# Optimization experiments

Measured on AMD Instinct MI355X. Metric: run time of the kernel, lower is better.

The kernel has to match this reference:

```python
import jax, jax.numpy as jnp
import numpy as np

B=4; TEXT_LEN=64; IMG=256; P=16; DIM=1024; HEADS=16; LAYERS=2; MLP=4; VOCAB=50000; TDIM=256; MAXTXT=2048
HP=IMG//P; NPATCH=HP*HP; HD=DIM//HEADS; EPS=1e-5

def _ln(x, g, b):
    m = jnp.mean(x, -1, keepdims=True)
    v = jnp.mean((x - m) ** 2, -1, keepdims=True)
    return (x - m) / jnp.sqrt(v + EPS) * g + b

def _rope_cos_sin(n, d):
    inv = 1.0 / (10000.0 ** (jnp.arange(0, d, 2, dtype=jnp.float32) / d))
    f = jnp.outer(jnp.arange(n, dtype=jnp.float32), inv)
    e = jnp.concatenate([f, f], -1)  # [n, d]
    return jnp.cos(e), jnp.sin(e)

def _rot_half(x):
    # matches torch: cat((-x[...,1::2], x[...,::2]), -1)
    return jnp.concatenate([-x[..., 1::2], x[..., ::2]], -1)

def _forward(noisy_images, text_tokens, timesteps, W_tok, pos_text, W_patch, pos_img, cls_tok,
             W_t1, b_t1, W_t2, b_t2, ln1_g, ln1_b, Wq, Wk, Wv, Wo, ln2_g, ln2_b,
             Wm1, Wm2, Wada, b_ada, fn_g, fn_b, W_final, b_final):
    Bn = noisy_images.shape[0]
    # text embed: one_hot @ W_tok.T == gather of columns of W_tok [DIM, VOCAB]
    text_emb = jnp.transpose(jnp.take(W_tok, text_tokens, axis=1), (1, 2, 0)) + pos_text[:, :TEXT_LEN]
    # image patches: [B,3,HP,P,HP,P] -> [B,HP,WP,C,P,P] -> [B,NPATCH, 3*P*P]
    patches = noisy_images.reshape(Bn, 3, HP, P, HP, P).transpose(0, 2, 4, 1, 3, 5).reshape(Bn, NPATCH, 3 * P * P)
    img_emb = patches @ W_patch.T + pos_img
    img_emb = jnp.concatenate([jnp.broadcast_to(cls_tok, (Bn, 1, DIM)), img_emb], 1)
    x = jnp.concatenate([text_emb, img_emb], 1)  # [B, N, DIM]
    N = x.shape[1]
    # sinusoidal timestep embedding (dim=256)
    half = TDIM // 2
    freqs = jnp.exp(-jnp.log(10000.0) * jnp.arange(half, dtype=jnp.float32) / half)
    args = timesteps.astype(jnp.float32)[:, None] * freqs[None]
    temb_raw = jnp.concatenate([jnp.cos(args), jnp.sin(args)], -1)
    t_emb = jax.nn.silu(temb_raw @ W_t1.T + b_t1) @ W_t2.T + b_t2  # [B, DIM]
    cos, sin = _rope_cos_sin(N, HD)
    scale = HD ** -0.5
    for l in range(LAYERS):
        mod = jax.nn.silu(t_emb) @ Wada[l].T + b_ada[l]
        sh_msa, sc_msa, g_msa, sh_mlp, sc_mlp, g_mlp = jnp.split(mod, 6, -1)
        xn = _ln(x, ln1_g[l], ln1_b[l]) * (1 + sc_msa[:, None]) + sh_msa[:, None]
        q = (xn @ Wq[l].T).reshape(Bn, N, HEADS, HD).transpose(0, 2, 1, 3)
        k = (xn @ Wk[l].T).reshape(Bn, N, HEADS, HD).transpose(0, 2, 1, 3)
        v = (xn @ Wv[l].T).reshape(Bn, N, HEADS, HD).transpose(0, 2, 1, 3)
        q = q * cos + _rot_half(q) * sin
        k = k * cos + _rot_half(k) * sin
        att = jax.nn.softmax(jnp.einsum('bhnd,bhmd->bhnm', q, k) * scale, -1)
        o = jnp.einsum('bhnm,bhmd->bhnd', att, v).transpose(0, 2, 1, 3).reshape(Bn, N, DIM)
        x = x + g_msa[:, None] * (o @ Wo[l].T)
        xn2 = _ln(x, ln2_g[l], ln2_b[l]) * (1 + sc_mlp[:, None]) + sh_mlp[:, None]
        mlp = jax.nn.gelu(xn2 @ Wm1[l].T, approximate=False) @ Wm2[l].T
        x = x + g_mlp[:, None] * mlp
    img_tok = x[:, TEXT_LEN + 1:]
    out = _ln(img_tok, fn_g, fn_b) @ W_final.T + b_final  # [B, NPATCH, 3*P*P]
    out = out.reshape(Bn, HP, HP, 3, P, P).transpose(0, 3, 1, 4, 2, 5).reshape(Bn, 3, IMG, IMG)
    return out

def setup_inputs() -> dict:
    key = jax.random.key(0)
    ks = jax.random.split(key, 24)
    def n(k, shape, s=0.02):
        return (jax.random.normal(k, shape, jnp.float32) * s).astype(jnp.float32)
    inp = {}
    inp['noisy_images'] = jax.random.normal(ks[0], (B, 3, IMG, IMG), jnp.float32)
    inp['text_tokens'] = jax.random.randint(ks[1], (B, TEXT_LEN), 0, VOCAB)
    inp['timesteps'] = jax.random.randint(ks[2], (B,), 0, 1000)
    inp['W_tok'] = n(ks[3], (DIM, VOCAB))
    inp['pos_text'] = n(ks[4], (1, MAXTXT, DIM))
    inp['W_patch'] = n(ks[5], (DIM, 3 * P * P))
    inp['pos_img'] = n(ks[6], (1, NPATCH, DIM))
    inp['cls_tok'] = n(ks[7], (1, 1, DIM))
    inp['W_t1'] = n(ks[8], (DIM, TDIM)); inp['b_t1'] = jnp.zeros((DIM,), jnp.float32)
    inp['W_t2'] = n(ks[9], (DIM, DIM)); inp['b_t2'] = jnp.zeros((DIM,), jnp.float32)
    inp['ln1_g'] = jnp.ones((LAYERS, DIM), jnp.float32); inp['ln1_b'] = jnp.zeros((LAYERS, DIM), jnp.float32)
    inp['Wq'] = n(ks[10], (LAYERS, DIM, DIM))
    inp['Wk'] = n(ks[11], (LAYERS, DIM, DIM))
    inp['Wv'] = n(ks[12], (LAYERS, DIM, DIM))
    inp['Wo'] = n(ks[13], (LAYERS, DIM, DIM))
    inp['ln2_g'] = jnp.ones((LAYERS, DIM), jnp.float32); inp['ln2_b'] = jnp.zeros((LAYERS, DIM), jnp.float32)
    inp['Wm1'] = n(ks[14], (LAYERS, MLP * DIM, DIM))
    inp['Wm2'] = n(ks[15], (LAYERS, DIM, MLP * DIM))
    inp['Wada'] = n(ks[16], (LAYERS, 6 * DIM, DIM)); inp['b_ada'] = jnp.zeros((LAYERS, 6 * DIM), jnp.float32)
    inp['fn_g'] = jnp.ones((DIM,), jnp.float32); inp['fn_b'] = jnp.zeros((DIM,), jnp.float32)
    inp['W_final'] = n(ks[17], (3 * P * P, DIM)); inp['b_final'] = jnp.zeros((3 * P * P,), jnp.float32)
    return inp

def reference(noisy_images, text_tokens, timesteps, W_tok, pos_text, W_patch, pos_img, cls_tok,
              W_t1, b_t1, W_t2, b_t2, ln1_g, ln1_b, Wq, Wk, Wv, Wo, ln2_g, ln2_b,
              Wm1, Wm2, Wada, b_ada, fn_g, fn_b, W_final, b_final):
    return _forward(noisy_images, text_tokens, timesteps, W_tok, pos_text, W_patch, pos_img, cls_tok,
                    W_t1, b_t1, W_t2, b_t2, ln1_g, ln1_b, Wq, Wk, Wv, Wo, ln2_g, ln2_b,
                    Wm1, Wm2, Wada, b_ada, fn_g, fn_b, W_final, b_final)
```

## Files before the change

### kernel.cpp

```cpp
#include <hip/hip_runtime.h>
#include <math.h>

constexpr int kBn    = 4;
constexpr int kText  = 64;
constexpr int kImg   = 256;
constexpr int kDim   = 1024;
constexpr int kHeads = 16;
constexpr int kHd    = 64;
constexpr int kNp    = 256;
constexpr int kTok   = 321;
constexpr int kVocab = 50000;
constexpr int kTdim  = 256;
constexpr int kMlp   = 4096;
constexpr int kScLd  = 328;
constexpr float kEps = 1e-5f;

typedef __attribute__((ext_vector_type(8))) short short8;
typedef __attribute__((ext_vector_type(4))) float f32x4;

__device__ __forceinline__ short f2bf(float x) {
  unsigned u = __builtin_bit_cast(unsigned, x);
  unsigned r = (u + 0x7FFFu + ((u >> 16) & 1u)) >> 16;
  return (short)r;
}

__device__ __forceinline__ void glds16(const short* g, short* l) {
  __builtin_amdgcn_global_load_lds(
      (const __attribute__((address_space(1))) unsigned int*)g,
      (__attribute__((address_space(3))) unsigned int*)l, 16, 0, 0);
}

struct GemmM {
  const short* A; const short* B; float* C; const float* E;
  int M, N, K, lda, ldb, ldc;
  long sA0, sA1, sB0, sB1, sC0, sC1;
  int innerB, ldE, rowsPB;
  float alpha;
  int nSplit, splitLen;
  long partStride;
};

__device__ __forceinline__ float epi_apply(int EPI, const GemmM& p, const float* E,
                                           long co, int gm, int gn, float v) {
  if (EPI == 1) v += E[gn];
  else if (EPI == 3) v = 0.5f*v*(1.f + erff(v*0.70710678118654752f));
  else if (EPI == 4) v += E[(long)gm*p.ldE + gn];
  else if (EPI == 5) v = p.C[co] + E[(long)(gm / p.rowsPB)*p.ldE + gn] * v;
  return v;
}

template<int EPI, bool PART, bool OUTBF>
__global__ __launch_bounds__(256) void gemm_gl(GemmM p) {
  int bz = blockIdx.z;
  int split = 0;
  if (PART) { split = bz % p.nSplit; bz /= p.nSplit; }
  int b1 = bz % p.innerB, b0 = bz / p.innerB;
  const short* A = p.A + b0*p.sA0 + b1*p.sA1;
  const short* B = p.B + b0*p.sB0 + b1*p.sB1;
  long cbase = b0*p.sC0 + b1*p.sC1 + (PART ? (long)split * p.partStride : 0);
  const float* E = p.E;

  int kBeg = PART ? split * p.splitLen : 0;
  int kEnd = PART ? min(p.K, kBeg + p.splitLen) : p.K;

  __shared__ short As[2][64*64];
  __shared__ short Bs[2][64*64];

  int tid  = threadIdx.x;
  int lane = tid & 63, widx = tid >> 6;
  int quad = lane >> 4, ln = lane & 15;
  int wm = (widx >> 1) * 32, wn = (widx & 1) * 32;
  int n0 = blockIdx.x * 64, m0 = blockIdx.y * 64;

  int l3 = lane >> 3, l7 = lane & 7;
  int kofs = (l7 ^ l3) * 8;
  const short* gA0 = A + (long)(m0 + 16*widx + l3) * p.lda + kofs;
  const short* gA1 = gA0 + (long)8 * p.lda;
  const short* gB0 = B + (long)(n0 + 16*widx + l3) * p.ldb + kofs;
  const short* gB1 = gB0 + (long)8 * p.ldb;
  short* lA0 = &As[0][(2*widx)*512];
  short* lA1 = &As[0][(2*widx+1)*512];
  short* lB0 = &Bs[0][(2*widx)*512];
  short* lB1 = &Bs[0][(2*widx+1)*512];

  auto stage = [&](int buf, int k0) {
    int bo = buf * 4096;
    glds16(gA0 + k0, lA0 + bo);
    glds16(gA1 + k0, lA1 + bo);
    glds16(gB0 + k0, lB0 + bo);
    glds16(gB1 + k0, lB1 + bo);
  };

  f32x4 zero = {0.f, 0.f, 0.f, 0.f};
  f32x4 acc[2][2];
  acc[0][0] = zero; acc[0][1] = zero; acc[1][0] = zero; acc[1][1] = zero;

  stage(0, kBeg);
  int buf = 0;
  for (int k0 = kBeg; k0 < kEnd; k0 += 64) {
    if (k0 + 64 < kEnd) stage(buf ^ 1, k0 + 64);
    __syncthreads();
    const char* Ab = (const char*)&As[buf][0];
    const char* Bb = (const char*)&Bs[buf][0];
#pragma unroll
    for (int ks = 0; ks < 2; ++ks) {
      int cb = ks*64 + quad*16;
      int r0 = wm + ln, r1 = wm + 16 + ln, r2 = wn + ln, r3 = wn + 16 + ln;
      short8 a0 = *(const short8*)(Ab + r0*128 + (cb ^ ((r0 & 7) << 4)));
      short8 a1 = *(const short8*)(Ab + r1*128 + (cb ^ ((r1 & 7) << 4)));
      short8 b0 = *(const short8*)(Bb + r2*128 + (cb ^ ((r2 & 7) << 4)));
      short8 b1 = *(const short8*)(Bb + r3*128 + (cb ^ ((r3 & 7) << 4)));
      acc[0][0] = __builtin_amdgcn_mfma_f32_16x16x32_bf16(a0, b0, acc[0][0], 0, 0, 0);
      acc[0][1] = __builtin_amdgcn_mfma_f32_16x16x32_bf16(a0, b1, acc[0][1], 0, 0, 0);
      acc[1][0] = __builtin_amdgcn_mfma_f32_16x16x32_bf16(a1, b0, acc[1][0], 0, 0, 0);
      acc[1][1] = __builtin_amdgcn_mfma_f32_16x16x32_bf16(a1, b1, acc[1][1], 0, 0, 0);
    }
    __syncthreads();
    buf ^= 1;
  }

#pragma unroll
  for (int mi = 0; mi < 2; ++mi)
#pragma unroll
    for (int ni = 0; ni < 2; ++ni)
#pragma unroll
      for (int reg = 0; reg < 4; ++reg) {
        int gm = m0 + wm + mi*16 + quad*4 + reg;
        int gn = n0 + wn + ni*16 + ln;
        if (gm >= p.M || gn >= p.N) continue;
        long co = cbase + (long)gm * p.ldc + gn;
        float v = acc[mi][ni][reg] * p.alpha;
        if (!PART) v = epi_apply(EPI, p, E, co, gm, gn, v);
        if (OUTBF) ((short*)p.C)[co] = f2bf(v);
        else       p.C[co] = v;
      }
}

template<int EPI, bool OUTBF>
__global__ __launch_bounds__(256) void gemm_mfma(GemmM p) {
  int bz = blockIdx.z;
  int b1 = bz % p.innerB, b0 = bz / p.innerB;
  const short* A = p.A + b0*p.sA0 + b1*p.sA1;
  const short* B = p.B + b0*p.sB0 + b1*p.sB1;
  long cbase = b0*p.sC0 + b1*p.sC1;
  const float* E = p.E;
  int kEnd = p.K;

  __shared__ short As[64*72];
  __shared__ short Bs[64*72];

  int tid  = threadIdx.x;
  int lane = tid & 63, widx = tid >> 6;
  int quad = lane >> 4, ln = lane & 15;
  int wm = (widx >> 1) * 32, wn = (widx & 1) * 32;
  int n0 = blockIdx.x * 64, m0 = blockIdx.y * 64;

  f32x4 zero = {0.f, 0.f, 0.f, 0.f};
  f32x4 acc[2][2];
  acc[0][0] = zero; acc[0][1] = zero; acc[1][0] = zero; acc[1][1] = zero;

  short8 ra[2], rb[2];
  auto issueLoads = [&](int k0) {
#pragma unroll
    for (int r = 0; r < 2; ++r) {
      int c = tid + 256*r;
      int row = c >> 3, kc = c & 7;
      int gk = k0 + kc*8;
      {
        int gm = m0 + row;
        const short* src = A + (long)gm * p.lda + gk;
        if (gm < p.M && gk + 8 <= kEnd) ra[r] = *(const short8*)src;
        else {
          short8 t = {0,0,0,0,0,0,0,0};
          if (gm < p.M) {
#pragma unroll
            for (int j = 0; j < 8; ++j) if (gk + j < kEnd) t[j] = src[j];
          }
          ra[r] = t;
        }
      }
      {
        int gn = n0 + row;
        const short* src = B + (long)gn * p.ldb + gk;
        if (gn < p.N && gk + 8 <= kEnd) rb[r] = *(const short8*)src;
        else {
          short8 t = {0,0,0,0,0,0,0,0};
          if (gn < p.N) {
#pragma unroll
            for (int j = 0; j < 8; ++j) if (gk + j < kEnd) t[j] = src[j];
          }
          rb[r] = t;
        }
      }
    }
  };

  issueLoads(0);
  for (int k0 = 0; k0 < kEnd; k0 += 64) {
#pragma unroll
    for (int r = 0; r < 2; ++r) {
      int c = tid + 256*r;
      int row = c >> 3, kc = c & 7;
      *(short8*)&As[row*72 + kc*8] = ra[r];
      *(short8*)&Bs[row*72 + kc*8] = rb[r];
    }
    __syncthreads();
    if (k0 + 64 < kEnd) issueLoads(k0 + 64);
#pragma unroll
    for (int ks = 0; ks < 2; ++ks) {
      short8 a0 = *(const short8*)&As[(wm +      ln)*72 + ks*32 + quad*8];
      short8 a1 = *(const short8*)&As[(wm + 16 + ln)*72 + ks*32 + quad*8];
      short8 b0 = *(const short8*)&Bs[(wn +      ln)*72 + ks*32 + quad*8];
      short8 b1 = *(const short8*)&Bs[(wn + 16 + ln)*72 + ks*32 + quad*8];
      acc[0][0] = __builtin_amdgcn_mfma_f32_16x16x32_bf16(a0, b0, acc[0][0], 0, 0, 0);
      acc[0][1] = __builtin_amdgcn_mfma_f32_16x16x32_bf16(a0, b1, acc[0][1], 0, 0, 0);
      acc[1][0] = __builtin_amdgcn_mfma_f32_16x16x32_bf16(a1, b0, acc[1][0], 0, 0, 0);
      acc[1][1] = __builtin_amdgcn_mfma_f32_16x16x32_bf16(a1, b1, acc[1][1], 0, 0, 0);
    }
    __syncthreads();
  }

#pragma unroll
  for (int mi = 0; mi < 2; ++mi)
#pragma unroll
    for (int ni = 0; ni < 2; ++ni)
#pragma unroll
      for (int reg = 0; reg < 4; ++reg) {
        int gm = m0 + wm + mi*16 + quad*4 + reg;
        int gn = n0 + wn + ni*16 + ln;
        if (gm >= p.M || gn >= p.N) continue;
        long co = cbase + (long)gm * p.ldc + gn;
        float v = acc[mi][ni][reg] * p.alpha;
        v = epi_apply(EPI, p, E, co, gm, gn, v);
        if (OUTBF) ((short*)p.C)[co] = f2bf(v);
        else       p.C[co] = v;
      }
}

static GemmM mkm(const short* A, const short* B, float* C,
                 int M, int N, int K, int lda, int ldb, int ldc) {
  GemmM p; p.A = A; p.B = B; p.C = C; p.E = nullptr;
  p.M = M; p.N = N; p.K = K; p.lda = lda; p.ldb = ldb; p.ldc = ldc;
  p.sA0 = p.sA1 = p.sB0 = p.sB1 = p.sC0 = p.sC1 = 0;
  p.innerB = 1; p.ldE = 0; p.rowsPB = 1; p.alpha = 1.f;
  p.nSplit = 1; p.splitLen = 0; p.partStride = 0;
  return p;
}

static void run_gl(hipStream_t s, int epi, bool outbf, const GemmM& p, int nb) {
  dim3 g((p.N + 63)/64, (p.M + 63)/64, nb), b(256, 1, 1);
  if (outbf) {
    if (epi == 3) gemm_gl<3,false,true><<<g,b,0,s>>>(p);
    else          gemm_gl<0,false,true><<<g,b,0,s>>>(p);
    return;
  }
  switch (epi) {
    case 0: gemm_gl<0,false,false><<<g,b,0,s>>>(p); break;
    case 1: gemm_gl<1,false,false><<<g,b,0,s>>>(p); break;
    case 4: gemm_gl<4,false,false><<<g,b,0,s>>>(p); break;
    case 5: gemm_gl<5,false,false><<<g,b,0,s>>>(p); break;
  }
}

static void run_gl_part(hipStream_t s, const GemmM& p, int nb) {
  dim3 g((p.N + 63)/64, (p.M + 63)/64, nb * p.nSplit), b(256, 1, 1);
  gemm_gl<0,true,false><<<g,b,0,s>>>(p);
}

static void run_pv(hipStream_t s, const GemmM& p, int nb) {
  dim3 g((p.N + 63)/64, (p.M + 63)/64, nb), b(256, 1, 1);
  gemm_mfma<0,true><<<g,b,0,s>>>(p);
}

__global__ __launch_bounds__(256) void reduce_epi4(
    const float* __restrict__ part, long partStride, int S,
    float* __restrict__ C, const float* __restrict__ E,
    int Mv, int Nv, int ldc, long sC0, int ldE, int total) {
  int idx = blockIdx.x*256 + threadIdx.x;
  if (idx >= total) return;
  int n = idx % Nv;
  int m = (idx / Nv) % Mv;
  int b0 = idx / (Nv * Mv);
  long co = b0*sC0 + (long)m*ldc + n;
  float v = 0.f;
  for (int s = 0; s < S; ++s) v += part[(long)s*partStride + co];
  v += E[(long)m*ldE + n];
  C[co] = v;
}

__global__ __launch_bounds__(256) void cvt2_bf16(const float* __restrict__ src,
                                                 short* __restrict__ dst, int n8,
                                                 long srcStride, long dstStride, int total8) {
  int i = blockIdx.x*256 + threadIdx.x;
  if (i >= total8) return;
  int l = i / n8, j = i % n8;
  const float* s = src + srcStride*l + (long)8*j;
  short* d = dst + dstStride*l + (long)8*j;
  float4 a = *(const float4*)s;
  float4 b = *(const float4*)(s + 4);
  short8 o;
  o[0]=f2bf(a.x); o[1]=f2bf(a.y); o[2]=f2bf(a.z); o[3]=f2bf(a.w);
  o[4]=f2bf(b.x); o[5]=f2bf(b.y); o[6]=f2bf(b.z); o[7]=f2bf(b.w);
  *(short8*)d = o;
}

static void cvtT(hipStream_t s, const float* src, short* dst, long nPerLayer,
                 long srcStride, long dstStride, int L) {
  int n8 = (int)(nPerLayer / 8);
  int total8 = n8 * L;
  cvt2_bf16<<<dim3((total8 + 255)/256), dim3(256), 0, s>>>(src, dst, n8, srcStride, dstStride, total8);
}

template<int EPI>
__global__ __launch_bounds__(256) void gemv4(const float* __restrict__ A,
                                             const float* __restrict__ B,
                                             float* __restrict__ C,
                                             const float* __restrict__ bias,
                                             int N, int K, int ldc) {
  int wave = threadIdx.x >> 6, lane = threadIdx.x & 63;
  int n = blockIdx.x * 4 + wave;
  if (n >= N) return;
  const float* Brow = B + (long)n * K;
  float acc0 = 0.f, acc1 = 0.f, acc2 = 0.f, acc3 = 0.f;
  for (int k = lane * 4; k < K; k += 256) {
    float4 b = *(const float4*)(Brow + k);
    float4 a0 = *(const float4*)(A + 0*K + k);
    float4 a1 = *(const float4*)(A + 1*K + k);
    float4 a2 = *(const float4*)(A + 2*K + k);
    float4 a3 = *(const float4*)(A + 3*K + k);
    acc0 += a0.x*b.x + a0.y*b.y + a0.z*b.z + a0.w*b.w;
    acc1 += a1.x*b.x + a1.y*b.y + a1.z*b.z + a1.w*b.w;
    acc2 += a2.x*b.x + a2.y*b.y + a2.z*b.z + a2.w*b.w;
    acc3 += a3.x*b.x + a3.y*b.y + a3.z*b.z + a3.w*b.w;
  }
#pragma unroll
  for (int off = 32; off; off >>= 1) {
    acc0 += __shfl_xor(acc0, off);
    acc1 += __shfl_xor(acc1, off);
    acc2 += __shfl_xor(acc2, off);
    acc3 += __shfl_xor(acc3, off);
  }
  if (lane == 0) {
    float bs = bias[n];
    float v[4] = {acc0 + bs, acc1 + bs, acc2 + bs, acc3 + bs};
#pragma unroll
    for (int m = 0; m < 4; ++m) {
      float x = v[m];
      if (EPI == 2) x = x / (1.f + expf(-x));
      C[(long)m * ldc + n] = x;
    }
  }
}

__global__ void embed_text_cls(const float* __restrict__ Wtok, const int* __restrict__ toks,
                               const float* __restrict__ pos_text, const float* __restrict__ cls_tok,
                               float* __restrict__ x) {
  int idx = blockIdx.x*256 + threadIdx.x;
  int d = idx % kDim;
  int t = (idx / kDim) % (kText + 1);
  int b = idx / (kDim * (kText + 1));
  float v;
  if (t < kText) {
    int tok = toks[b*kText + t];
    v = Wtok[(long)d*kVocab + tok] + pos_text[(long)t*kDim + d];
  } else {
    v = cls_tok[d];
  }
  x[((long)b*kTok + t)*kDim + d] = v;
}

__global__ void extract_patches(const float* __restrict__ img, short* __restrict__ pat) {
  int idx = blockIdx.x*256 + threadIdx.x;
  int k = idx % 768;
  int p = (idx/768) % kNp;
  int b = idx/(768*kNp);
  int c = k >> 8, py = (k >> 4) & 15, px = k & 15;
  int hp = p >> 4, wp = p & 15;
  pat[idx] = f2bf(img[(((long)(b*3 + c))*kImg + hp*16 + py)*kImg + wp*16 + px]);
}

__global__ void time_freqs(const int* __restrict__ ts, float* __restrict__ temb) {
  int b = blockIdx.x, i = threadIdx.x;
  float f = expf(-9.210340371976184f * (float)i / 128.f);
  float a = (float)ts[b] * f;
  temb[b*kTdim + i] = cosf(a);
  temb[b*kTdim + 128 + i] = sinf(a);
}

__global__ void silu_kernel(const float* __restrict__ in, float* __restrict__ outp, int n) {
  int i = blockIdx.x*256 + threadIdx.x;
  if (i < n) { float x = in[i]; outp[i] = x / (1.f + expf(-x)); }
}

__device__ __forceinline__ float block_sum(float v) {
  __shared__ float sh[4];
  for (int off = 32; off; off >>= 1) v += __shfl_down(v, off);
  if ((threadIdx.x & 63) == 0) sh[threadIdx.x >> 6] = v;
  __syncthreads();
  float s = sh[0] + sh[1] + sh[2] + sh[3];
  __syncthreads();
  return s;
}

__global__ __launch_bounds__(256) void ln_mod_kernel(
    const float* __restrict__ x, const float* __restrict__ g, const float* __restrict__ be,
    const float* __restrict__ mod, int shOff, int scOff, short* __restrict__ outp) {
  int row = blockIdx.x;
  int b = row / kTok;
  const float* xr = x + (long)row*kDim;
  float s = 0.f, s2 = 0.f;
  for (int i = threadIdx.x; i < kDim; i += 256) { float v = xr[i]; s += v; s2 += v*v; }
  s = block_sum(s); s2 = block_sum(s2);
  float m = s / kDim;
  float inv = rsqrtf(s2 / kDim - m*m + kEps);
  const float* mb = mod + (long)b*(6*kDim);
  for (int i = threadIdx.x; i < kDim; i += 256) {
    float xn = (xr[i] - m)*inv*g[i] + be[i];
    outp[(long)row*kDim + i] = f2bf(xn*(1.f + mb[scOff + i]) + mb[shOff + i]);
  }
}

__global__ __launch_bounds__(256) void ln_mod_red_kernel(
    const float* __restrict__ xin, const float* __restrict__ part, long pStride, int S,
    const float* __restrict__ gate, const float* __restrict__ g, const float* __restrict__ be,
    const float* __restrict__ mod, int shOff, int scOff,
    float* __restrict__ xout, short* __restrict__ outp) {
  int row = blockIdx.x;
  int b = row / kTok;
  long base = (long)row*kDim;
  const float* gt = gate + (long)b*(6*kDim);
  float v[4];
  float s = 0.f, s2 = 0.f;
#pragma unroll
  for (int c = 0; c < 4; ++c) {
    int i = threadIdx.x + 256*c;
    float acc = 0.f;
    for (int sp = 0; sp < S; ++sp) acc += part[(long)sp*pStride + base + i];
    float xv = xin[base + i] + gt[i] * acc;
    v[c] = xv; s += xv; s2 += xv*xv;
  }
  s = block_sum(s); s2 = block_sum(s2);
  float m = s / kDim;
  float inv = rsqrtf(s2 / kDim - m*m + kEps);
  const float* mb = mod + (long)b*(6*kDim);
#pragma unroll
  for (int c = 0; c < 4; ++c) {
    int i = threadIdx.x + 256*c;
    xout[base + i] = v[c];
    float xn = (v[c] - m)*inv*g[i] + be[i];
    outp[base + i] = f2bf(xn*(1.f + mb[scOff + i]) + mb[shOff + i]);
  }
}

__global__ __launch_bounds__(256) void final_ln_kernel(
    const float* __restrict__ x, const float* __restrict__ g, const float* __restrict__ be,
    short* __restrict__ yn) {
  int row = blockIdx.x;
  int b = row / kNp, p = row % kNp;
  const float* xr = x + ((long)(b*kTok + kText + 1 + p))*kDim;
  float s = 0.f, s2 = 0.f;
  for (int i = threadIdx.x; i < kDim; i += 256) { float v = xr[i]; s += v; s2 += v*v; }
  s = block_sum(s); s2 = block_sum(s2);
  float m = s / kDim;
  float inv = rsqrtf(s2 / kDim - m*m + kEps);
  for (int i = threadIdx.x; i < kDim; i += 256)
    yn[(long)row*kDim + i] = f2bf((xr[i] - m)*inv*g[i] + be[i]);
}

__global__ __launch_bounds__(256) void final_ln_red_kernel(
    const float* __restrict__ xin, const float* __restrict__ part, long pStride, int S,
    const float* __restrict__ gate, const float* __restrict__ g, const float* __restrict__ be,
    short* __restrict__ yn) {
  int row = blockIdx.x;
  int b = row / kNp, p = row % kNp;
  long xb = ((long)(b*kTok + kText + 1 + p))*kDim;
  const float* gt = gate + (long)b*(6*kDim);
  float v[4];
  float s = 0.f, s2 = 0.f;
#pragma unroll
  for (int c = 0; c < 4; ++c) {
    int i = threadIdx.x + 256*c;
    float acc = 0.f;
    for (int sp = 0; sp < S; ++sp) acc += part[(long)sp*pStride + xb + i];
    float xv = xin[xb + i] + gt[i] * acc;
    v[c] = xv; s += xv; s2 += xv*xv;
  }
  s = block_sum(s); s2 = block_sum(s2);
  float m = s / kDim;
  float inv = rsqrtf(s2 / kDim - m*m + kEps);
#pragma unroll
  for (int c = 0; c < 4; ++c) {
    int i = threadIdx.x + 256*c;
    yn[(long)row*kDim + i] = f2bf((v[c] - m)*inv*g[i] + be[i]);
  }
}

__global__ __launch_bounds__(256) void rope_bf16(const float* __restrict__ qkv,
                                                 short* __restrict__ qb,
                                                 short* __restrict__ kb) {
  int idx = blockIdx.x*256 + threadIdx.x;
  int d = idx & (kDim - 1);
  int r = idx >> 10;
  int n = r % kTok;
  int hd = d & 63;
  int j = hd & 31;
  float inv = expf(-9.210340371976184f * (float)j / 32.f);
  float ang = (float)n * inv;
  float c = cosf(ang), s = sinf(ang);
  const float* row = qkv + (long)r * (3*kDim);
  int base = d - hd;
  float qv = row[d], kv = row[kDim + d];
  float qr, kr;
  if (hd < 32) { qr = -row[base + 2*hd + 1];      kr = -row[kDim + base + 2*hd + 1]; }
  else         { qr =  row[base + 2*(hd - 32)];   kr =  row[kDim + base + 2*(hd - 32)]; }
  qb[idx] = f2bf(qv*c + qr*s);
  kb[idx] = f2bf(kv*c + kr*s);
}

__global__ __launch_bounds__(256) void vtrans_kernel(const float* __restrict__ qkv,
                                                     short* __restrict__ vtb) {
  int idx = blockIdx.x*256 + threadIdx.x;
  int tok = idx % kScLd;
  int hd  = (idx / kScLd) % kHd;
  int h   = (idx / (kScLd*kHd)) % kHeads;
  int b   = idx / (kScLd*kHd*kHeads);
  float v = 0.f;
  if (tok < kTok) v = qkv[((long)(b*kTok + tok))*(3*kDim) + 2*kDim + h*kHd + hd];
  vtb[idx] = f2bf(v);
}

__global__ __launch_bounds__(256) void softmax_rows4(float* __restrict__ sc,
                                                     short* __restrict__ dst, int nRows) {
  int wid = threadIdx.x >> 6, t = threadIdx.x & 63;
  int row = blockIdx.x*4 + wid;
  if (row >= nRows) return;
  float* r = sc + (long)row*kScLd;
  short* d = dst + (long)row*kScLd;
  float mx = -1e30f;
  for (int i = t; i < kTok; i += 64) mx = fmaxf(mx, r[i]);
  for (int off = 32; off; off >>= 1) mx = fmaxf(mx, __shfl_xor(mx, off));
  float sum = 0.f;
  for (int i = t; i < kTok; i += 64) { float e = expf(r[i] - mx); r[i] = e; sum += e; }
  for (int off = 32; off; off >>= 1) sum += __shfl_xor(sum, off);
  float invs = 1.f / sum;
  for (int i = t; i < kTok; i += 64) d[i] = f2bf(r[i] * invs);
}

__global__ void unpatchify(const float* __restrict__ op, float* __restrict__ outp) {
  int idx = blockIdx.x*256 + threadIdx.x;
  int w = idx & 255;
  int h = (idx >> 8) & 255;
  int c = (idx >> 16) % 3;
  int b = idx / (3 * kImg * kImg);
  int hp = h >> 4, py = h & 15, wp = w >> 4, px = w & 15;
  outp[idx] = op[((long)(b*kNp + hp*16 + wp))*768 + c*256 + py*16 + px];
}

__global__ void unpatchify_red(const float* __restrict__ part, long pStride, int S,
                               const float* __restrict__ bias, float* __restrict__ outp) {
  int idx = blockIdx.x*256 + threadIdx.x;
  int w = idx & 255;
  int h = (idx >> 8) & 255;
  int c = (idx >> 16) % 3;
  int b = idx / (3 * kImg * kImg);
  int hp = h >> 4, py = h & 15, wp = w >> 4, px = w & 15;
  long co = ((long)(b*kNp + hp*16 + wp))*768 + c*256 + py*16 + px;
  float v = bias[c*256 + py*16 + px];
  for (int s = 0; s < S; ++s) v += part[(long)s*pStride + co];
  outp[idx] = v;
}

extern "C" void kernel_launch(void* const* d_in, const int* in_sizes, int n_in,
                              void* d_out, int out_size, void* d_ws, size_t ws_size,
                              hipStream_t stream) {
  (void)in_sizes; (void)n_in; (void)out_size;
  const float* noisy    = (const float*)d_in[0];
  const int*   toks     = (const int*)d_in[1];
  const int*   tsteps   = (const int*)d_in[2];
  const float* W_tok    = (const float*)d_in[3];
  const float* pos_text = (const float*)d_in[4];
  const float* W_patch  = (const float*)d_in[5];
  const float* pos_img  = (const float*)d_in[6];
  const float* cls_tok  = (const float*)d_in[7];
  const float* W_t1     = (const float*)d_in[8];
  const float* b_t1     = (const float*)d_in[9];
  const float* W_t2     = (const float*)d_in[10];
  const float* b_t2     = (const float*)d_in[11];
  const float* ln1_g    = (const float*)d_in[12];
  const float* ln1_b    = (const float*)d_in[13];
  const float* Wq       = (const float*)d_in[14];
  const float* Wk       = (const float*)d_in[15];
  const float* Wv       = (const float*)d_in[16];
  const float* Wo       = (const float*)d_in[17];
  const float* ln2_g    = (const float*)d_in[18];
  const float* ln2_b    = (const float*)d_in[19];
  const float* Wm1      = (const float*)d_in[20];
  const float* Wm2      = (const float*)d_in[21];
  const float* Wada     = (const float*)d_in[22];
  const float* b_ada    = (const float*)d_in[23];
  const float* fn_g     = (const float*)d_in[24];
  const float* fn_b     = (const float*)d_in[25];
  const float* W_final  = (const float*)d_in[26];
  const float* b_final  = (const float*)d_in[27];
  float* out = (float*)d_out;

  float* ws = (float*)d_ws;
  auto alloc = [&](long nf) { float* r = ws; ws += nf; return r; };

  const long seqSz = (long)kBn * kTok * kDim;
  float* x    = alloc(seqSz);
  float* qkv  = alloc((long)kBn*kTok*3*kDim);
  float* sc   = alloc((long)kBn*kHeads*kTok*kScLd);
  short* xnb  = (short*)alloc(seqSz/2);
  short* qb   = (short*)alloc(seqSz/2);
  short* kb   = (short*)alloc(seqSz/2);
  short* ob   = (short*)alloc(seqSz/2);
  short* vtb  = (short*)alloc((long)kBn*kHeads*kHd*kScLd/2);
  short* scb  = (short*)alloc((long)kBn*kHeads*kTok*kScLd/2);
  short* patb = (short*)alloc((long)kBn*kNp*768/2);
  short* ynb  = (short*)alloc((long)kBn*kNp*kDim/2);
  float* temb = alloc(kBn*kTdim);
  float* t1   = alloc(kBn*kDim);
  float* temb2= alloc(kBn*kDim);
  float* st   = alloc(kBn*kDim);
  float* mod  = alloc(2L*kBn*6*kDim);
  short* hb   = (short*)sc;
  float* outp = qkv;

  const long oPatch = 0;
  const long nPatch = (long)kDim*768;
  const long perLayer = 3L*kDim*kDim + (long)kDim*kDim + 2L*kMlp*kDim;
  const long oLayer = nPatch;
  const long oFinal = nPatch + 2*perLayer;
  const long nFinal = (long)768*kDim;
  short* wAr = (short*)alloc((nPatch + 2*perLayer + nFinal)/2);

  const long scrStride = seqSz;
  float* scr = alloc(4*scrStride);
  bool split_ok = ((char*)ws - (char*)d_ws) <= (long)ws_size;

  cvtT(stream, W_patch, wAr + oPatch, nPatch, 0, 0, 1);
  cvtT(stream, Wq,  wAr + oLayer + 0,               (long)kDim*kDim, (long)kDim*kDim, perLayer, 2);
  cvtT(stream, Wk,  wAr + oLayer + (long)kDim*kDim, (long)kDim*kDim, (long)kDim*kDim, perLayer, 2);
  cvtT(stream, Wv,  wAr + oLayer + 2L*kDim*kDim,    (long)kDim*kDim, (long)kDim*kDim, perLayer, 2);
  cvtT(stream, Wo,  wAr + oLayer + 3L*kDim*kDim,    (long)kDim*kDim, (long)kDim*kDim, perLayer, 2);
  cvtT(stream, Wm1, wAr + oLayer + 4L*kDim*kDim,    (long)kMlp*kDim, (long)kMlp*kDim, perLayer, 2);
  cvtT(stream, Wm2, wAr + oLayer + 4L*kDim*kDim + (long)kMlp*kDim,
       (long)kMlp*kDim, (long)kMlp*kDim, perLayer, 2);
  cvtT(stream, W_final, wAr + oFinal, nFinal, 0, 0, 1);

  embed_text_cls<<<(kBn*(kText+1)*kDim)/256, 256, 0, stream>>>(W_tok, toks, pos_text, cls_tok, x);
  extract_patches<<<(kBn*kNp*768)/256, 256, 0, stream>>>(noisy, patb);
  {
    GemmM p = mkm(patb, wAr + oPatch, split_ok ? scr : (x + (kText+1)*kDim),
                  kNp, kDim, 768, 768, 768, kDim);
    p.sA0 = (long)kNp*768; p.sC0 = (long)kTok*kDim;
    if (split_ok) {
      p.nSplit = 3; p.splitLen = 256; p.partStride = scrStride;
      run_gl_part(stream, p, kBn);
      int total = kBn*kNp*kDim;
      reduce_epi4<<<(total+255)/256, 256, 0, stream>>>(scr, scrStride, 3,
          x + (kText+1)*kDim, pos_img, kNp, kDim, kDim, (long)kTok*kDim, kDim, total);
    } else {
      p.E = pos_img; p.ldE = kDim;
      run_gl(stream, 4, false, p, kBn);
    }
  }
  time_freqs<<<kBn, 128, 0, stream>>>(tsteps, temb);
  gemv4<2><<<kDim/4, 256, 0, stream>>>(temb, W_t1, t1, b_t1, kDim, kTdim, kDim);
  gemv4<1><<<kDim/4, 256, 0, stream>>>(t1, W_t2, temb2, b_t2, kDim, kDim, kDim);
  silu_kernel<<<(kBn*kDim + 255)/256, 256, 0, stream>>>(temb2, st, kBn*kDim);
  for (int l = 0; l < 2; ++l)
    gemv4<1><<<(6*kDim)/4, 256, 0, stream>>>(st, Wada + (long)l*6*kDim*kDim,
                                             mod + (long)l*kBn*6*kDim,
                                             b_ada + (long)l*6*kDim, 6*kDim, kDim, 6*kDim);

  ln_mod_kernel<<<kBn*kTok, 256, 0, stream>>>(x, ln1_g, ln1_b, mod, 0, kDim, xnb);

  for (int l = 0; l < 2; ++l) {
    const short* wqkv_l = wAr + oLayer + (long)l*perLayer;
    const short* wo_l   = wqkv_l + 3L*kDim*kDim;
    const short* wm1_l  = wqkv_l + 4L*kDim*kDim;
    const short* wm2_l  = wm1_l + (long)kMlp*kDim;
    float* mod_l = mod + (long)l*kBn*6*kDim;

    {
      GemmM p = mkm(xnb, wqkv_l, qkv, kBn*kTok, 3*kDim, kDim, kDim, kDim, 3*kDim);
      run_gl(stream, 0, false, p, 1);
    }
    rope_bf16<<<(int)(seqSz/256), 256, 0, stream>>>(qkv, qb, kb);
    vtrans_kernel<<<(kBn*kHeads*kHd*kScLd)/256, 256, 0, stream>>>(qkv, vtb);

    {
      GemmM p = mkm(qb, kb, sc, kTok, kTok, kHd, kDim, kDim, kScLd);
      p.sA0 = (long)kTok*kDim; p.sA1 = kHd;
      p.sB0 = (long)kTok*kDim; p.sB1 = kHd;
      p.sC0 = (long)kHeads*kTok*kScLd; p.sC1 = (long)kTok*kScLd;
      p.innerB = kHeads; p.alpha = 0.125f;
      run_gl(stream, 0, false, p, kBn*kHeads);
    }
    {
      int nRows = kBn*kHeads*kTok;
      softmax_rows4<<<(nRows+3)/4, 256, 0, stream>>>(sc, scb, nRows);
    }
    {
      GemmM p = mkm(scb, vtb, (float*)ob, kTok, kHd, kTok, kScLd, kScLd, kDim);
      p.sA0 = (long)kHeads*kTok*kScLd; p.sA1 = (long)kTok*kScLd;
      p.sB0 = (long)kHeads*kHd*kScLd;  p.sB1 = (long)kHd*kScLd;
      p.sC0 = (long)kTok*kDim;         p.sC1 = kHd;
      p.innerB = kHeads;
      run_pv(stream, p, kBn*kHeads);
    }
    {
      GemmM p = mkm(ob, wo_l, split_ok ? scr : x, kBn*kTok, kDim, kDim, kDim, kDim, kDim);
      if (split_ok) {
        p.nSplit = 4; p.splitLen = 256; p.partStride = scrStride;
        run_gl_part(stream, p, 1);
        ln_mod_red_kernel<<<kBn*kTok, 256, 0, stream>>>(x, scr, scrStride, 4,
            mod_l + 2*kDim, ln2_g + l*kDim, ln2_b + l*kDim, mod_l, 3*kDim, 4*kDim, x, xnb);
      } else {
        p.E = mod_l + 2*kDim; p.ldE = 6*kDim; p.rowsPB = kTok;
        run_gl(stream, 5, false, p, 1);
        ln_mod_kernel<<<kBn*kTok, 256, 0, stream>>>(x, ln2_g + l*kDim, ln2_b + l*kDim,
                                                    mod_l, 3*kDim, 4*kDim, xnb);
      }
    }
    {
      GemmM p = mkm(xnb, wm1_l, (float*)hb, kBn*kTok, kMlp, kDim, kDim, kDim, kMlp);
      run_gl(stream, 3, true, p, 1);
    }
    {
      GemmM p = mkm(hb, wm2_l, split_ok ? scr : x, kBn*kTok, kDim, kMlp, kMlp, kMlp, kDim);
      if (split_ok) {
        p.nSplit = 4; p.splitLen = 1024; p.partStride = scrStride;
        run_gl_part(stream, p, 1);
        if (l == 0) {
          ln_mod_red_kernel<<<kBn*kTok, 256, 0, stream>>>(x, scr, scrStride, 4,
              mod_l + 5*kDim, ln1_g + kDim, ln1_b + kDim,
              mod + (long)kBn*6*kDim, 0, kDim, x, xnb);
        } else {
          final_ln_red_kernel<<<kBn*kNp, 256, 0, stream>>>(x, scr, scrStride, 4,
              mod_l + 5*kDim, fn_g, fn_b, ynb);
        }
      } else {
        p.E = mod_l + 5*kDim; p.ldE = 6*kDim; p.rowsPB = kTok;
        run_gl(stream, 5, false, p, 1);
        if (l == 0)
          ln_mod_kernel<<<kBn*kTok, 256, 0, stream>>>(x, ln1_g + kDim, ln1_b + kDim,
                                                      mod + (long)kBn*6*kDim, 0, kDim, xnb);
        else
          final_ln_kernel<<<kBn*kNp, 256, 0, stream>>>(x, fn_g, fn_b, ynb);
      }
    }
  }

  {
    GemmM p = mkm(ynb, wAr + oFinal, split_ok ? scr : outp, kBn*kNp, 768, kDim, kDim, kDim, 768);
    if (split_ok) {
      p.nSplit = 4; p.splitLen = 256; p.partStride = (long)kBn*kNp*768;
      run_gl_part(stream, p, 1);
      unpatchify_red<<<(kBn*3*kImg*kImg)/256, 256, 0, stream>>>(scr, (long)kBn*kNp*768, 4,
                                                                b_final, out);
    } else {
      p.E = b_final;
      run_gl(stream, 1, false, p, 1);
      unpatchify<<<(kBn*3*kImg*kImg)/256, 256, 0, stream>>>(outp, out);
    }
  }
}
```

Before: 790.5 us.

## Add double-buffered 64x128 swizzled GEMM tile and pad attention PV path

Adds a GEMM kernel with a 64x128 output tile. It stages A and B through double-buffered XOR-swizzled LDS using direct global-to-LDS loads, so each warp computes 4x2 MFMA tiles with more reuse and fewer register round-trips. All dense projections (QKV, Wo, MLP, patch, final) now use it. The V transpose now goes through an LDS tile, and the softmax output is padded to 384 rows and columns so the PV product can use the generic unchecked-load GEMM. The new loads skip per-row bounds checks, so for the M=1284 case they can read past the last row. Padding also adds extra K work in PV.

```diff
diff --git a/kernel.cpp b/kernel.cpp
--- a/kernel.cpp
+++ b/kernel.cpp
@@ -12,7 +12,8 @@
 constexpr int kVocab = 50000;
 constexpr int kTdim  = 256;
 constexpr int kMlp   = 4096;
-constexpr int kScLd  = 328;
+constexpr int kScLd  = 384;
+constexpr int kScRow = 384;
 constexpr float kEps = 1e-5f;
 
 typedef __attribute__((ext_vector_type(8))) short short8;
@@ -136,102 +137,95 @@
       }
 }
 
-template<int EPI, bool OUTBF>
-__global__ __launch_bounds__(256) void gemm_mfma(GemmM p) {
+template<int EPI, bool PART, bool OUTBF>
+__global__ __launch_bounds__(256) void gemm_gl_n128(GemmM p) {
   int bz = blockIdx.z;
+  int split = 0;
+  if (PART) { split = bz % p.nSplit; bz /= p.nSplit; }
   int b1 = bz % p.innerB, b0 = bz / p.innerB;
   const short* A = p.A + b0*p.sA0 + b1*p.sA1;
   const short* B = p.B + b0*p.sB0 + b1*p.sB1;
-  long cbase = b0*p.sC0 + b1*p.sC1;
+  long cbase = b0*p.sC0 + b1*p.sC1 + (PART ? (long)split * p.partStride : 0);
   const float* E = p.E;
-  int kEnd = p.K;
-
-  __shared__ short As[64*72];
-  __shared__ short Bs[64*72];
+
+  int kBeg = PART ? split * p.splitLen : 0;
+  int kEnd = PART ? min(p.K, kBeg + p.splitLen) : p.K;
+
+  __shared__ short As[2][64*64];
+  __shared__ short Bs[2][128*64];
 
   int tid  = threadIdx.x;
   int lane = tid & 63, widx = tid >> 6;
   int quad = lane >> 4, ln = lane & 15;
-  int wm = (widx >> 1) * 32, wn = (widx & 1) * 32;
-  int n0 = blockIdx.x * 64, m0 = blockIdx.y * 64;
+  int n0 = blockIdx.x * 128, m0 = blockIdx.y * 64;
+
+  int l3 = lane >> 3, l7 = lane & 7;
+  int kofs = (l7 ^ l3) * 8;
+  const short* gA0 = A + (long)(m0 + 16*widx + l3) * p.lda + kofs;
+  const short* gA1 = gA0 + (long)8 * p.lda;
+  const short* gB0 = B + (long)(n0 + 32*widx + l3) * p.ldb + kofs;
+  const long ldb8 = (long)8 * p.ldb;
+  short* lA = &As[0][(2*widx)*512];
+  short* lB = &Bs[0][(4*widx)*512];
+
+  auto stage = [&](int buf, int k0) {
+    int boA = buf * 4096, boB = buf * 8192;
+    glds16(gA0 + k0, lA + boA);
+    glds16(gA1 + k0, lA + 512 + boA);
+    glds16(gB0 + k0,            lB + boB);
+    glds16(gB0 + ldb8 + k0,     lB + 512 + boB);
+    glds16(gB0 + 2*ldb8 + k0,   lB + 1024 + boB);
+    glds16(gB0 + 3*ldb8 + k0,   lB + 1536 + boB);
+  };
 
   f32x4 zero = {0.f, 0.f, 0.f, 0.f};
-  f32x4 acc[2][2];
-  acc[0][0] = zero; acc[0][1] = zero; acc[1][0] = zero; acc[1][1] = zero;
-
-  short8 ra[2], rb[2];
-  auto issueLoads = [&](int k0) {
-#pragma unroll
-    for (int r = 0; r < 2; ++r) {
-      int c = tid + 256*r;
-      int row = c >> 3, kc = c & 7;
-      int gk = k0 + kc*8;
-      {
-        int gm = m0 + row;
-        const short* src = A + (long)gm * p.lda + gk;
-        if (gm < p.M && gk + 8 <= kEnd) ra[r] = *(const short8*)src;
-        else {
-          short8 t = {0,0,0,0,0,0,0,0};
-          if (gm < p.M) {
-#pragma unroll
-            for (int j = 0; j < 8; ++j) if (gk + j < kEnd) t[j] = src[j];
-          }
-          ra[r] = t;
-        }
+  f32x4 acc[4][2];
+#pragma unroll
+  for (int i = 0; i < 4; ++i) { acc[i][0] = zero; acc[i][1] = zero; }
+
+  stage(0, kBeg);
+  int buf = 0;
+  for (int k0 = kBeg; k0 < kEnd; k0 += 64) {
+    if (k0 + 64 < kEnd) stage(buf ^ 1, k0 + 64);
+    __syncthreads();
+    const char* Ab = (const char*)&As[buf][0];
+    const char* Bb = (const char*)&Bs[buf][0];
+#pragma unroll
+    for (int ks = 0; ks < 2; ++ks) {
+      int cb = ks*64 + quad*16;
+      short8 a[4], b[2];
+#pragma unroll
+      for (int mi = 0; mi < 4; ++mi) {
+        int r = mi*16 + ln;
+        a[mi] = *(const short8*)(Ab + r*128 + (cb ^ ((r & 7) << 4)));
       }
-      {
-        int gn = n0 + row;
-        const short* src = B + (long)gn * p.ldb + gk;
-        if (gn < p.N && gk + 8 <= kEnd) rb[r] = *(const short8*)src;
-        else {
-          short8 t = {0,0,0,0,0,0,0,0};
-          if (gn < p.N) {
-#pragma unroll
-            for (int j = 0; j < 8; ++j) if (gk + j < kEnd) t[j] = src[j];
-          }
-          rb[r] = t;
-        }
+#pragma unroll
+      for (int ni = 0; ni < 2; ++ni) {
+        int r = 32*widx + ni*16 + ln;
+        b[ni] = *(const short8*)(Bb + r*128 + (cb ^ ((r & 7) << 4)));
       }
-    }
-  };
-
-  issueLoads(0);
-  for (int k0 = 0; k0 < kEnd; k0 += 64) {
-#pragma unroll
-    for (int r = 0; r < 2; ++r) {
-      int c = tid + 256*r;
-      int row = c >> 3, kc = c & 7;
-      *(short8*)&As[row*72 + kc*8] = ra[r];
-      *(short8*)&Bs[row*72 + kc*8] = rb[r];
+#pragma unroll
+      for (int mi = 0; mi < 4; ++mi)
+#pragma unroll
+        for (int ni = 0; ni < 2; ++ni)
+          acc[mi][ni] = __builtin_amdgcn_mfma_f32_16x16x32_bf16(a[mi], b[ni], acc[mi][ni], 0, 0, 0);
     }
     __syncthreads();
-    if (k0 + 64 < kEnd) issueLoads(k0 + 64);
-#pragma unroll
-    for (int ks = 0; ks < 2; ++ks) {
-      short8 a0 = *(const short8*)&As[(wm +      ln)*72 + ks*32 + quad*8];
-      short8 a1 = *(const short8*)&As[(wm + 16 + ln)*72 + ks*32 + quad*8];
-      short8 b0 = *(const short8*)&Bs[(wn +      ln)*72 + ks*32 + quad*8];
-      short8 b1 = *(const short8*)&Bs[(wn + 16 + ln)*72 + ks*32 + quad*8];
-      acc[0][0] = __builtin_amdgcn_mfma_f32_16x16x32_bf16(a0, b0, acc[0][0], 0, 0, 0);
-      acc[0][1] = __builtin_amdgcn_mfma_f32_16x16x32_bf16(a0, b1, acc[0][1], 0, 0, 0);
-      acc[1][0] = __builtin_amdgcn_mfma_f32_16x16x32_bf16(a1, b0, acc[1][0], 0, 0, 0);
-      acc[1][1] = __builtin_amdgcn_mfma_f32_16x16x32_bf16(a1, b1, acc[1][1], 0, 0, 0);
-    }
-    __syncthreads();
-  }
-
-#pragma unroll
-  for (int mi = 0; mi < 2; ++mi)
+    buf ^= 1;
+  }
+
+#pragma unroll
+  for (int mi = 0; mi < 4; ++mi)
 #pragma unroll
     for (int ni = 0; ni < 2; ++ni)
 #pragma unroll
       for (int reg = 0; reg < 4; ++reg) {
-        int gm = m0 + wm + mi*16 + quad*4 + reg;
-        int gn = n0 + wn + ni*16 + ln;
+        int gm = m0 + mi*16 + quad*4 + reg;
+        int gn = n0 + 32*widx + ni*16 + ln;
         if (gm >= p.M || gn >= p.N) continue;
         long co = cbase + (long)gm * p.ldc + gn;
         float v = acc[mi][ni][reg] * p.alpha;
-        v = epi_apply(EPI, p, E, co, gm, gn, v);
+        if (!PART) v = epi_apply(EPI, p, E, co, gm, gn, v);
         if (OUTBF) ((short*)p.C)[co] = f2bf(v);
         else       p.C[co] = v;
       }
@@ -262,14 +256,24 @@
   }
 }
 
-static void run_gl_part(hipStream_t s, const GemmM& p, int nb) {
-  dim3 g((p.N + 63)/64, (p.M + 63)/64, nb * p.nSplit), b(256, 1, 1);
-  gemm_gl<0,true,false><<<g,b,0,s>>>(p);
-}
-
-static void run_pv(hipStream_t s, const GemmM& p, int nb) {
-  dim3 g((p.N + 63)/64, (p.M + 63)/64, nb), b(256, 1, 1);
-  gemm_mfma<0,true><<<g,b,0,s>>>(p);
+static void run_gl128(hipStream_t s, int epi, bool outbf, const GemmM& p, int nb) {
+  dim3 g((p.N + 127)/128, (p.M + 63)/64, nb), b(256, 1, 1);
+  if (outbf) {
+    if (epi == 3) gemm_gl_n128<3,false,true><<<g,b,0,s>>>(p);
+    else          gemm_gl_n128<0,false,true><<<g,b,0,s>>>(p);
+    return;
+  }
+  switch (epi) {
+    case 0: gemm_gl_n128<0,false,false><<<g,b,0,s>>>(p); break;
+    case 1: gemm_gl_n128<1,false,false><<<g,b,0,s>>>(p); break;
+    case 4: gemm_gl_n128<4,false,false><<<g,b,0,s>>>(p); break;
+    case 5: gemm_gl_n128<5,false,false><<<g,b,0,s>>>(p); break;
+  }
+}
+
+static void run_gl128_part(hipStream_t s, const GemmM& p, int nb) {
+  dim3 g((p.N + 127)/128, (p.M + 63)/64, nb * p.nSplit), b(256, 1, 1);
+  gemm_gl_n128<0,true,false><<<g,b,0,s>>>(p);
 }
 
 __global__ __launch_bounds__(256) void reduce_epi4(
@@ -517,25 +521,39 @@
   kb[idx] = f2bf(kv*c + kr*s);
 }
 
-__global__ __launch_bounds__(256) void vtrans_kernel(const float* __restrict__ qkv,
-                                                     short* __restrict__ vtb) {
-  int idx = blockIdx.x*256 + threadIdx.x;
-  int tok = idx % kScLd;
-  int hd  = (idx / kScLd) % kHd;
-  int h   = (idx / (kScLd*kHd)) % kHeads;
-  int b   = idx / (kScLd*kHd*kHeads);
-  float v = 0.f;
-  if (tok < kTok) v = qkv[((long)(b*kTok + tok))*(3*kDim) + 2*kDim + h*kHd + hd];
-  vtb[idx] = f2bf(v);
+__global__ __launch_bounds__(256) void vtrans_t(const float* __restrict__ qkv,
+                                                short* __restrict__ vtb) {
+  int tt = blockIdx.x;
+  int bh = blockIdx.y;
+  int b = bh >> 4, h = bh & 15;
+  __shared__ float tile[64][65];
+  int t = threadIdx.x;
+#pragma unroll
+  for (int i = 0; i < 16; ++i) {
+    int idx = t + 256*i;
+    int tok = idx >> 6, d = idx & 63;
+    int gtok = tt*64 + tok;
+    float v = 0.f;
+    if (gtok < kTok) v = qkv[((long)(b*kTok + gtok))*(3*kDim) + 2*kDim + h*kHd + d];
+    tile[tok][d] = v;
+  }
+  __syncthreads();
+#pragma unroll
+  for (int i = 0; i < 16; ++i) {
+    int idx = t + 256*i;
+    int d = idx >> 6, tok = idx & 63;
+    vtb[((long)bh*kHd + d)*kScLd + tt*64 + tok] = f2bf(tile[tok][d]);
+  }
 }
 
 __global__ __launch_bounds__(256) void softmax_rows4(float* __restrict__ sc,
-                                                     short* __restrict__ dst, int nRows) {
+                                                     short* __restrict__ scb, int nRows) {
   int wid = threadIdx.x >> 6, t = threadIdx.x & 63;
   int row = blockIdx.x*4 + wid;
   if (row >= nRows) return;
   float* r = sc + (long)row*kScLd;
-  short* d = dst + (long)row*kScLd;
+  int bh = row / kTok, ri = row % kTok;
+  short* d = scb + (long)bh*kScRow*kScLd + (long)ri*kScLd;
   float mx = -1e30f;
   for (int i = t; i < kTok; i += 64) mx = fmaxf(mx, r[i]);
   for (int off = 32; off; off >>= 1) mx = fmaxf(mx, __shfl_xor(mx, off));
@@ -543,7 +561,8 @@
   for (int i = t; i < kTok; i += 64) { float e = expf(r[i] - mx); r[i] = e; sum += e; }
   for (int off = 32; off; off >>= 1) sum += __shfl_xor(sum, off);
   float invs = 1.f / sum;
-  for (int i = t; i < kTok; i += 64) d[i] = f2bf(r[i] * invs);
+  for (int i = t; i < kScLd; i += 64)
+    d[i] = (i < kTok) ? f2bf(r[i] * invs) : (short)0;
 }
 
 __global__ void unpatchify(const float* __restrict__ op, float* __restrict__ outp) {
@@ -616,7 +635,7 @@
   short* kb   = (short*)alloc(seqSz/2);
   short* ob   = (short*)alloc(seqSz/2);
   short* vtb  = (short*)alloc((long)kBn*kHeads*kHd*kScLd/2);
-  short* scb  = (short*)alloc((long)kBn*kHeads*kTok*kScLd/2);
+  short* scb  = (short*)alloc((long)kBn*kHeads*kScRow*kScLd/2);
   short* patb = (short*)alloc((long)kBn*kNp*768/2);
   short* ynb  = (short*)alloc((long)kBn*kNp*kDim/2);
   float* temb = alloc(kBn*kTdim);
@@ -657,13 +676,13 @@
     p.sA0 = (long)kNp*768; p.sC0 = (long)kTok*kDim;
     if (split_ok) {
       p.nSplit = 3; p.splitLen = 256; p.partStride = scrStride;
-      run_gl_part(stream, p, kBn);
+      run_gl128_part(stream, p, kBn);
       int total = kBn*kNp*kDim;
       reduce_epi4<<<(total+255)/256, 256, 0, stream>>>(scr, scrStride, 3,
           x + (kText+1)*kDim, pos_img, kNp, kDim, kDim, (long)kTok*kDim, kDim, total);
     } else {
       p.E = pos_img; p.ldE = kDim;
-      run_gl(stream, 4, false, p, kBn);
+      run_gl128(stream, 4, false, p, kBn);
     }
   }
   time_freqs<<<kBn, 128, 0, stream>>>(tsteps, temb);
@@ -686,10 +705,10 @@
 
     {
       GemmM p = mkm(xnb, wqkv_l, qkv, kBn*kTok, 3*kDim, kDim, kDim, kDim, 3*kDim);
-      run_gl(stream, 0, false, p, 1);
+      run_gl128(stream, 0, false, p, 1);
     }
     rope_bf16<<<(int)(seqSz/256), 256, 0, stream>>>(qkv, qb, kb);
-    vtrans_kernel<<<(kBn*kHeads*kHd*kScLd)/256, 256, 0, stream>>>(qkv, vtb);
+    vtrans_t<<<dim3(kScLd/64, kBn*kHeads), 256, 0, stream>>>(qkv, vtb);
 
     {
       GemmM p = mkm(qb, kb, sc, kTok, kTok, kHd, kDim, kDim, kScLd);
@@ -704,36 +723,36 @@
       softmax_rows4<<<(nRows+3)/4, 256, 0, stream>>>(sc, scb, nRows);
     }
     {
-      GemmM p = mkm(scb, vtb, (float*)ob, kTok, kHd, kTok, kScLd, kScLd, kDim);
-      p.sA0 = (long)kHeads*kTok*kScLd; p.sA1 = (long)kTok*kScLd;
-      p.sB0 = (long)kHeads*kHd*kScLd;  p.sB1 = (long)kHd*kScLd;
-      p.sC0 = (long)kTok*kDim;         p.sC1 = kHd;
+      GemmM p = mkm(scb, vtb, (float*)ob, kTok, kHd, kScLd, kScLd, kScLd, kDim);
+      p.sA0 = (long)kHeads*kScRow*kScLd; p.sA1 = (long)kScRow*kScLd;
+      p.sB0 = (long)kHeads*kHd*kScLd;    p.sB1 = (long)kHd*kScLd;
+      p.sC0 = (long)kTok*kDim;           p.sC1 = kHd;
       p.innerB = kHeads;
-      run_pv(stream, p, kBn*kHeads);
+      run_gl(stream, 0, true, p, kBn*kHeads);
     }
     {
       GemmM p = mkm(ob, wo_l, split_ok ? scr : x, kBn*kTok, kDim, kDim, kDim, kDim, kDim);
       if (split_ok) {
         p.nSplit = 4; p.splitLen = 256; p.partStride = scrStride;
-        run_gl_part(stream, p, 1);
+        run_gl128_part(stream, p, 1);
         ln_mod_red_kernel<<<kBn*kTok, 256, 0, stream>>>(x, scr, scrStride, 4,
             mod_l + 2*kDim, ln2_g + l*kDim, ln2_b + l*kDim, mod_l, 3*kDim, 4*kDim, x, xnb);
       } else {
         p.E = mod_l + 2*kDim; p.ldE = 6*kDim; p.rowsPB = kTok;
-        run_gl(stream, 5, false, p, 1);
+        run_gl128(stream, 5, false, p, 1);
         ln_mod_kernel<<<kBn*kTok, 256, 0, stream>>>(x, ln2_g + l*kDim, ln2_b + l*kDim,
                                                     mod_l, 3*kDim, 4*kDim, xnb);
       }
     }
     {
       GemmM p = mkm(xnb, wm1_l, (float*)hb, kBn*kTok, kMlp, kDim, kDim, kDim, kMlp);
-      run_gl(stream, 3, true, p, 1);
+      run_gl128(stream, 3, true, p, 1);
     }
     {
       GemmM p = mkm(hb, wm2_l, split_ok ? scr : x, kBn*kTok, kDim, kMlp, kMlp, kMlp, kDim);
       if (split_ok) {
         p.nSplit = 4; p.splitLen = 1024; p.partStride = scrStride;
-        run_gl_part(stream, p, 1);
+        run_gl128_part(stream, p, 1);
         if (l == 0) {
           ln_mod_red_kernel<<<kBn*kTok, 256, 0, stream>>>(x, scr, scrStride, 4,
               mod_l + 5*kDim, ln1_g + kDim, ln1_b + kDim,
@@ -744,7 +763,7 @@
         }
       } else {
         p.E = mod_l + 5*kDim; p.ldE = 6*kDim; p.rowsPB = kTok;
-        run_gl(stream, 5, false, p, 1);
+        run_gl128(stream, 5, false, p, 1);
         if (l == 0)
           ln_mod_kernel<<<kBn*kTok, 256, 0, stream>>>(x, ln1_g + kDim, ln1_b + kDim,
                                                       mod + (long)kBn*6*kDim, 0, kDim, xnb);
@@ -758,12 +777,12 @@
     GemmM p = mkm(ynb, wAr + oFinal, split_ok ? scr : outp, kBn*kNp, 768, kDim, kDim, kDim, 768);
     if (split_ok) {
       p.nSplit = 4; p.splitLen = 256; p.partStride = (long)kBn*kNp*768;
-      run_gl_part(stream, p, 1);
+      run_gl128_part(stream, p, 1);
       unpatchify_red<<<(kBn*3*kImg*kImg)/256, 256, 0, stream>>>(scr, (long)kBn*kNp*768, 4,
                                                                 b_final, out);
     } else {
       p.E = b_final;
-      run_gl(stream, 1, false, p, 1);
+      run_gl128(stream, 1, false, p, 1);
       unpatchify<<<(kBn*3*kImg*kImg)/256, 256, 0, stream>>>(outp, out);
     }
   }
```

New measurement: 786.6 us. About the same (-0.5%).
